# Kernel tuning notes

Measured on AMD Instinct MI355X. Metric: run time of the kernel, lower is better.

Reference implementation:

```python
import jax, jax.numpy as jnp
import numpy as np

B, T, N, H = 4096, 128, 128, 128  # batch, timesteps, input_size, encoder_num_hidden
EPS = 1e-5  # BatchNorm1d eps


def setup_inputs() -> dict:
    key = jax.random.key(0)
    ks = jax.random.split(key, 12)
    g = lambda k, shp, s=0.088: jax.random.normal(k, shp, dtype=jnp.float32) * s  # ~1/sqrt(H)
    return {
        "X": jax.random.normal(ks[0], (B, T, N), dtype=jnp.float32),
        "attn_w": g(ks[1], (2 * H + T,)),
        "attn_b": jnp.zeros((), jnp.float32),
        "bn_gamma": jnp.ones((N,), jnp.float32),
        "bn_beta": jnp.zeros((N,), jnp.float32),
        "W_ih0": g(ks[2], (4 * H, N)),
        "W_hh0": g(ks[3], (4 * H, H)),
        "b_ih0": g(ks[4], (4 * H,)),
        "b_hh0": g(ks[5], (4 * H,)),
        "W_ih1": g(ks[6], (4 * H, H)),
        "W_hh1": g(ks[7], (4 * H, H)),
        "b_ih1": g(ks[8], (4 * H,)),
        "b_hh1": g(ks[9], (4 * H,)),
    }


def _lstm_cell(x, h, c, W_ih, W_hh, b):
    # torch gate order: i, f, g, o
    gates = x @ W_ih.T + h @ W_hh.T + b  # (B, 4H)
    i, f, gg, o = jnp.split(gates, 4, axis=-1)
    c_new = jax.nn.sigmoid(f) * c + jax.nn.sigmoid(i) * jnp.tanh(gg)
    h_new = jax.nn.sigmoid(o) * jnp.tanh(c_new)
    return h_new, c_new


def reference(X, attn_w, attn_b, bn_gamma, bn_beta,
              W_ih0, W_hh0, b_ih0, b_hh0, W_ih1, W_hh1, b_ih1, b_hh1):
    # Attention input per step is cat(h_top repeat, s_top repeat, X^T) -> Linear(2H+T -> 1).
    # The X^T contribution is time-invariant; precompute it once.
    w_h, w_s, w_x = attn_w[:H], attn_w[H:2 * H], attn_w[2 * H:]
    Xp = jnp.transpose(X, (0, 2, 1))            # (B, N, T) driving-series view
    score_x = Xp @ w_x + attn_b                 # (B, N)
    b0 = b_ih0 + b_hh0
    b1 = b_ih1 + b_hh1

    def step(carry, x_t):
        h0, c0, h1, c1 = carry                  # layer0/layer1 hidden & cell (B, H)
        # h_n[-1], s_n[-1] are broadcast identically over all N features
        scores = score_x + (h1 @ w_h)[:, None] + (c1 @ w_s)[:, None]  # (B, N)
        alpha = jax.nn.softmax(scores, axis=1)
        x_tilde = alpha * x_t                   # (B, N)
        # BatchNorm1d in training mode: batch statistics over dim 0
        mean = jnp.mean(x_tilde, axis=0)
        var = jnp.var(x_tilde, axis=0)
        xb = (x_tilde - mean) * jax.lax.rsqrt(var + EPS) * bn_gamma + bn_beta
        # 2-layer LSTM single step (dropout inactive in eval)
        h0n, c0n = _lstm_cell(xb, h0, c0, W_ih0, W_hh0, b0)
        h1n, c1n = _lstm_cell(h0n, h1, c1, W_ih1, W_hh1, b1)
        return (h0n, c0n, h1n, c1n), (x_tilde, h1n)

    zeros = jnp.zeros((B, H), X.dtype)
    init = (zeros, zeros, zeros, zeros)
    Xt = jnp.transpose(X, (1, 0, 2))            # (T, B, N) for scan
    _, (xt_seq, he_seq) = jax.lax.scan(step, init, Xt)
    X_tilde = jnp.transpose(xt_seq, (1, 0, 2))   # (B, T, N)
    X_encoded = jnp.transpose(he_seq, (1, 0, 2)) # (B, T, H)
    return X_tilde, X_encoded
```

## Files before the change

### kernel.cpp

```cpp
#include <hip/hip_runtime.h>
#include <cstdint>
#include <cstddef>

#define B_ 4096
#define T_ 128
#define N_ 128
#define H_ 128
#define G4_ 512
#define KC_ 256
#define EPS_ 1e-5f

#define RPB_ 16
#define NB_ 256
#define W0K_ 128
#define W0P_ 136

#define KB2_ 256
#define ROWS2_ 16

typedef _Float16 f16x8 __attribute__((ext_vector_type(8)));
typedef _Float16 f16x4 __attribute__((ext_vector_type(4)));
typedef float f32x4 __attribute__((ext_vector_type(4)));

__device__ __forceinline__ float sigm_(float x) { return 1.f / (1.f + __expf(-x)); }
__device__ __forceinline__ float tanh_(float x) {
  float ax = fabsf(x);
  float e = __expf(-2.f * ax);
  float t = (1.f - e) / (1.f + e);
  return copysignf(t, x);
}

__global__ void k0_prep(const float* __restrict__ Wih0, const float* __restrict__ Whh0,
                        const float* __restrict__ bih0, const float* __restrict__ bhh0,
                        const float* __restrict__ Wih1, const float* __restrict__ Whh1,
                        const float* __restrict__ bih1, const float* __restrict__ bhh1,
                        _Float16* __restrict__ Wpack, float* __restrict__ bpack) {
  int idx = blockIdx.x * blockDim.x + threadIdx.x;
  if (idx < 2 * G4_ * KC_) {
    int k = idx & (KC_ - 1);
    int j = (idx >> 8) & (G4_ - 1);
    int l = idx >> 17;
    const float* Wih = l ? Wih1 : Wih0;
    const float* Whh = l ? Whh1 : Whh0;
    float v = (k < N_) ? Wih[j * N_ + k] : Whh[j * N_ + (k - N_)];
    Wpack[idx] = (_Float16)v;
  }
  if (idx < 2 * G4_) {
    int j = idx & (G4_ - 1);
    bpack[idx] = (idx >> 9) ? (bih1[j] + bhh1[j]) : (bih0[j] + bhh0[j]);
  }
}

__global__ __launch_bounds__(512, 1) void k12_fused(
    const float* __restrict__ X, const float* __restrict__ attn_w,
    const float* __restrict__ attn_b, float* __restrict__ out0,
    float* __restrict__ psum, float* __restrict__ psq) {
  __shared__ float xs[2 * T_ * N_];
  __shared__ float wx[T_];
  __shared__ float redS[4][N_];
  __shared__ float redM[8], redE[8];
  const int tid = threadIdx.x;
  const int blk = blockIdx.x;
  const int n = tid & 127;
  const int tq = tid >> 7;
  const int wv = tid >> 6;
  const int row0 = blk * ROWS2_;
  if (tid < T_) wx[tid] = attn_w[2 * H_ + tid];
  const float ab = attn_b[0];

  float sum[32], sq[32];
#pragma unroll
  for (int i = 0; i < 32; ++i) { sum[i] = 0.f; sq[i] = 0.f; }

  {
    const float* xb = X + (size_t)row0 * T_ * N_;
#pragma unroll
    for (int i = 0; i < 8; ++i) {
      int fi = ((i << 9) + tid) << 2;
      *(f32x4*)&xs[fi] = *(const f32x4*)&xb[fi];
    }
  }

  int buf = 0;
  for (int rb = 0; rb < ROWS2_; ++rb) {
    __syncthreads();
    const float* xcur = xs + (buf << 14);

    f32x4 stg[8];
    if (rb + 1 < ROWS2_) {
      const float* xb1 = X + (size_t)(row0 + rb + 1) * T_ * N_;
#pragma unroll
      for (int i = 0; i < 8; ++i)
        stg[i] = *(const f32x4*)&xb1[((i << 9) + tid) << 2];
    }

    float s = 0.f;
#pragma unroll
    for (int tt = 0; tt < 32; ++tt) {
      int t = (tq << 5) + tt;
      s = fmaf(xcur[t * N_ + n], wx[t], s);
    }
    redS[tq][n] = s;
    __syncthreads();
    s = redS[0][n] + redS[1][n] + redS[2][n] + redS[3][n] + ab;

    float m = s;
#pragma unroll
    for (int off = 32; off >= 1; off >>= 1) m = fmaxf(m, __shfl_xor(m, off));
    if ((tid & 63) == 0) redM[wv] = m;
    __syncthreads();
    m = fmaxf(fmaxf(fmaxf(redM[0], redM[1]), fmaxf(redM[2], redM[3])),
              fmaxf(fmaxf(redM[4], redM[5]), fmaxf(redM[6], redM[7])));
    float e = __expf(s - m);
    float sm = e;
#pragma unroll
    for (int off = 32; off >= 1; off >>= 1) sm += __shfl_xor(sm, off);
    if ((tid & 63) == 0) redE[wv] = sm;
    __syncthreads();
    sm = redE[0] + redE[1];
    const float alpha = e / sm;

    if (rb + 1 < ROWS2_) {
      float* xnx = xs + ((buf ^ 1) << 14);
#pragma unroll
      for (int i = 0; i < 8; ++i)
        *(f32x4*)&xnx[((i << 9) + tid) << 2] = stg[i];
    }

    const size_t b = (size_t)(row0 + rb);
#pragma unroll
    for (int tt = 0; tt < 32; ++tt) {
      int t = (tq << 5) + tt;
      float v = alpha * xcur[t * N_ + n];
      sum[tt] += v;
      sq[tt] += v * v;
      out0[(b * T_ + t) * N_ + n] = v;
    }
    buf ^= 1;
  }

  float* pbs = psum + ((size_t)blk << 14) + (tq << 5) * N_ + n;
  float* pbq = psq + ((size_t)blk << 14) + (tq << 5) * N_ + n;
#pragma unroll
  for (int tt = 0; tt < 32; ++tt) {
    pbs[tt * N_] = sum[tt];
    pbq[tt * N_] = sq[tt];
  }
}

__global__ void k3r(const float* __restrict__ psum, const float* __restrict__ psq,
                    const float* __restrict__ gamma, const float* __restrict__ beta,
                    float* __restrict__ scale, float* __restrict__ shift) {
  __shared__ float rs[2][N_], rq[2][N_];
  const int t = blockIdx.x;
  const int tid = threadIdx.x;
  const int n = tid & 127;
  const int hb = tid >> 7;
  const size_t off = (size_t)t * N_ + n;
  float s = 0.f, q = 0.f;
#pragma unroll 4
  for (int i = 0; i < 128; ++i) {
    size_t o = ((size_t)((hb << 7) + i) << 14) + off;
    s += psum[o];
    q += psq[o];
  }
  rs[hb][n] = s;
  rq[hb][n] = q;
  __syncthreads();
  if (hb == 0) {
    s = rs[0][n] + rs[1][n];
    q = rq[0][n] + rq[1][n];
    float mean = s * (1.f / B_);
    float var = q * (1.f / B_) - mean * mean;
    float rstd = rsqrtf(var + EPS_);
    float g = gamma[n];
    scale[t * N_ + n] = rstd * g;
    shift[t * N_ + n] = beta[n] - mean * rstd * g;
  }
}

__global__ __launch_bounds__(512, 2) void k4_recur(
    const float* __restrict__ xt , const _Float16* __restrict__ Wpack,
    const float* __restrict__ bpack, const float* __restrict__ scale,
    const float* __restrict__ shift, float* __restrict__ out1) {
  __shared__ _Float16 W0l[G4_][W0P_];
  __shared__ _Float16 A0[RPB_][264];
  __shared__ _Float16 A1[RPB_][264];

  const int tid = threadIdx.x;
  const int w = tid >> 6;
  const int lane = tid & 63;
  const int quad = lane >> 4;
  const int l16 = lane & 15;
  const int nb = blockIdx.x;
  const int col = (w << 4) + l16;

  {
    const _Float16* src = Wpack + (size_t)tid * KC_;
#pragma unroll
    for (int kk = 0; kk < W0K_; kk += 8)
      *(f16x8*)&W0l[tid][kk] = *(const f16x8*)&src[kk];
  }

  f16x8 w1[4][8];
#pragma unroll
  for (int g = 0; g < 4; ++g) {
    const _Float16* src = Wpack + (size_t)(G4_ + (g << 7) + col) * KC_ + (quad << 3);
#pragma unroll
    for (int kb = 0; kb < 8; ++kb) w1[g][kb] = *(const f16x8*)&src[kb << 5];
  }

  float bia0[4], bia1[4];
#pragma unroll
  for (int g = 0; g < 4; ++g) {
    bia0[g] = bpack[(g << 7) + col];
    bia1[g] = bpack[G4_ + (g << 7) + col];
  }

  float c0[4], c1[4];
#pragma unroll
  for (int e = 0; e < 4; ++e) { c0[e] = 0.f; c1[e] = 0.f; }

  const int sr = tid >> 5;
  const int sc = (tid & 31) << 2;
  const size_t browbase = (size_t)(nb * RPB_ + sr) * T_;

  {
    f32x4 xv = *(const f32x4*)(xt + (browbase + 0) * N_ + sc);
    f32x4 s4 = *(const f32x4*)(scale + sc);
    f32x4 h4 = *(const f32x4*)(shift + sc);
    f16x4 hv;
#pragma unroll
    for (int e = 0; e < 4; ++e) hv[e] = (_Float16)fmaf(xv[e], s4[e], h4[e]);
    *(f16x4*)&A0[sr][sc] = hv;
    f16x4 z = {};
    *(f16x4*)&A0[sr][N_ + sc] = z;
    *(f16x4*)&A1[sr][N_ + sc] = z;
  }
  __syncthreads();

  for (int t = 0; t < T_; ++t) {
    f32x4 xn = {};
    if (t + 1 < T_) xn = *(const f32x4*)(xt + (browbase + t + 1) * N_ + sc);

    f32x4 acc[4] = {};
#pragma unroll
    for (int kb = 0; kb < 8; ++kb) {
      f16x8 a = *(const f16x8*)&A0[l16][(kb << 5) + (quad << 3)];
      if (kb < 4) {
#pragma unroll
        for (int g = 0; g < 4; ++g) {
          f16x8 bf = *(const f16x8*)&W0l[(g << 7) + col][(kb << 5) + (quad << 3)];
          acc[g] = __builtin_amdgcn_mfma_f32_16x16x32_f16(a, bf, acc[g], 0, 0, 0);
        }
      } else {
#pragma unroll
        for (int g = 0; g < 4; ++g) {
          f16x8 bf = *(const f16x8*)(Wpack + (size_t)((g << 7) + col) * KC_ +
                                     (kb << 5) + (quad << 3));
          acc[g] = __builtin_amdgcn_mfma_f32_16x16x32_f16(a, bf, acc[g], 0, 0, 0);
        }
      }
    }

    _Float16 h0h[4];
#pragma unroll
    for (int e = 0; e < 4; ++e) {
      float ig = acc[0][e] + bia0[0];
      float fg = acc[1][e] + bia0[1];
      float gg = acc[2][e] + bia0[2];
      float og = acc[3][e] + bia0[3];
      float cn = sigm_(fg) * c0[e] + sigm_(ig) * tanh_(gg);
      c0[e] = cn;
      h0h[e] = (_Float16)(sigm_(og) * tanh_(cn));
    }
    __syncthreads();
#pragma unroll
    for (int e = 0; e < 4; ++e) {
      A0[(quad << 2) + e][N_ + col] = h0h[e];
      A1[(quad << 2) + e][col] = h0h[e];
    }
    __syncthreads();

    f16x8 a1[8];
#pragma unroll
    for (int kb = 0; kb < 4; ++kb) {
      a1[kb] = *(const f16x8*)&A1[l16][(kb << 5) + (quad << 3)];
      a1[4 + kb] = *(const f16x8*)&A1[l16][128 + (kb << 5) + (quad << 3)];
    }
    f32x4 acc1[4] = {};
#pragma unroll
    for (int kb = 0; kb < 8; ++kb) {
#pragma unroll
      for (int g = 0; g < 4; ++g)
        acc1[g] = __builtin_amdgcn_mfma_f32_16x16x32_f16(a1[kb], w1[g][kb], acc1[g], 0, 0, 0);
    }

    _Float16 h1h[4];
#pragma unroll
    for (int e = 0; e < 4; ++e) {
      float ig = acc1[0][e] + bia1[0];
      float fg = acc1[1][e] + bia1[1];
      float gg = acc1[2][e] + bia1[2];
      float og = acc1[3][e] + bia1[3];
      float cn = sigm_(fg) * c1[e] + sigm_(ig) * tanh_(gg);
      c1[e] = cn;
      float hn = sigm_(og) * tanh_(cn);
      h1h[e] = (_Float16)hn;
      out1[((size_t)(nb * RPB_ + (quad << 2) + e) * T_ + t) * H_ + col] = hn;
    }
    __syncthreads();
#pragma unroll
    for (int e = 0; e < 4; ++e)
      A1[(quad << 2) + e][N_ + col] = h1h[e];
    if (t + 1 < T_) {
      f32x4 s4 = *(const f32x4*)(scale + (t + 1) * N_ + sc);
      f32x4 h4 = *(const f32x4*)(shift + (t + 1) * N_ + sc);
      f16x4 hv;
#pragma unroll
      for (int e = 0; e < 4; ++e) hv[e] = (_Float16)fmaf(xn[e], s4[e], h4[e]);
      *(f16x4*)&A0[sr][sc] = hv;
    }
    __syncthreads();
  }
}

extern "C" void kernel_launch(void* const* d_in, const int* in_sizes, int n_in,
                              void* d_out, int out_size, void* d_ws, size_t ws_size,
                              hipStream_t stream) {
  const float* X = (const float*)d_in[0];
  const float* attnw = (const float*)d_in[1];
  const float* attnb = (const float*)d_in[2];
  const float* gamma = (const float*)d_in[3];
  const float* beta = (const float*)d_in[4];
  const float* Wih0 = (const float*)d_in[5];
  const float* Whh0 = (const float*)d_in[6];
  const float* bih0 = (const float*)d_in[7];
  const float* bhh0 = (const float*)d_in[8];
  const float* Wih1 = (const float*)d_in[9];
  const float* Whh1 = (const float*)d_in[10];
  const float* bih1 = (const float*)d_in[11];
  const float* bhh1 = (const float*)d_in[12];

  float* out0 = (float*)d_out;
  float* out1 = out0 + (size_t)B_ * T_ * N_;

  float* psum = out1;
  float* psq = out1 + ((size_t)KB2_ << 14);

  float* ws = (float*)d_ws;
  float* scale = ws;
  float* shift = scale + T_ * N_;
  float* bpack = shift + T_ * N_;
  _Float16* Wpack = (_Float16*)(bpack + 2 * G4_);

  k0_prep<<<1024, 256, 0, stream>>>(Wih0, Whh0, bih0, bhh0, Wih1, Whh1, bih1, bhh1,
                                    Wpack, bpack);
  k12_fused<<<KB2_, 512, 0, stream>>>(X, attnw, attnb, out0, psum, psq);
  k3r<<<T_, 256, 0, stream>>>(psum, psq, gamma, beta, scale, shift);
  k4_recur<<<NB_, 512, 0, stream>>>(out0, Wpack, bpack, scale, shift, out1);
}
```

Measured before the change: 1.332 ms.

## Software-pipeline LSTM layers so layer1 step t overlaps layer0 step t+1

Restructures the recurrent loop into a prologue, a steady-state loop and an epilogue. Layer-1 of step t and layer-0 of step t+1 now run in the same iteration, since they depend on the same h0 and on independent state. This halves the block barriers per timestep and gives the scheduler two independent MFMA chains to interleave, hiding MFMA and LDS latency. The cost is higher register pressure from holding two accumulator sets at once, plus a few extra prefetched loads.

```diff
diff --git a/kernel.cpp b/kernel.cpp
--- a/kernel.cpp
+++ b/kernel.cpp
@@ -29,6 +29,8 @@
   float t = (1.f - e) / (1.f + e);
   return copysignf(t, x);
 }
+
+#define MFMA16(a, b, c) __builtin_amdgcn_mfma_f32_16x16x32_f16((a), (b), (c), 0, 0, 0)
 
 __global__ void k0_prep(const float* __restrict__ Wih0, const float* __restrict__ Whh0,
                         const float* __restrict__ bih0, const float* __restrict__ bhh0,
@@ -224,6 +226,7 @@
   const int sr = tid >> 5;
   const int sc = (tid & 31) << 2;
   const size_t browbase = (size_t)(nb * RPB_ + sr) * T_;
+  const size_t orowbase = (size_t)(nb * RPB_ + (quad << 2)) * T_;
 
   {
     f32x4 xv = *(const f32x4*)(xt + (browbase + 0) * N_ + sc);
@@ -239,10 +242,7 @@
   }
   __syncthreads();
 
-  for (int t = 0; t < T_; ++t) {
-    f32x4 xn = {};
-    if (t + 1 < T_) xn = *(const f32x4*)(xt + (browbase + t + 1) * N_ + sc);
-
+  {
     f32x4 acc[4] = {};
 #pragma unroll
     for (int kb = 0; kb < 8; ++kb) {
@@ -251,18 +251,17 @@
 #pragma unroll
         for (int g = 0; g < 4; ++g) {
           f16x8 bf = *(const f16x8*)&W0l[(g << 7) + col][(kb << 5) + (quad << 3)];
-          acc[g] = __builtin_amdgcn_mfma_f32_16x16x32_f16(a, bf, acc[g], 0, 0, 0);
+          acc[g] = MFMA16(a, bf, acc[g]);
         }
       } else {
 #pragma unroll
         for (int g = 0; g < 4; ++g) {
           f16x8 bf = *(const f16x8*)(Wpack + (size_t)((g << 7) + col) * KC_ +
                                      (kb << 5) + (quad << 3));
-          acc[g] = __builtin_amdgcn_mfma_f32_16x16x32_f16(a, bf, acc[g], 0, 0, 0);
+          acc[g] = MFMA16(a, bf, acc[g]);
         }
       }
     }
-
     _Float16 h0h[4];
 #pragma unroll
     for (int e = 0; e < 4; ++e) {
@@ -277,10 +276,28 @@
     __syncthreads();
 #pragma unroll
     for (int e = 0; e < 4; ++e) {
+      A1[(quad << 2) + e][col] = h0h[e];
       A0[(quad << 2) + e][N_ + col] = h0h[e];
-      A1[(quad << 2) + e][col] = h0h[e];
-    }
-    __syncthreads();
+    }
+    {
+      f32x4 xv = *(const f32x4*)(xt + (browbase + 1) * N_ + sc);
+      f32x4 s4 = *(const f32x4*)(scale + 1 * N_ + sc);
+      f32x4 h4 = *(const f32x4*)(shift + 1 * N_ + sc);
+      f16x4 hv;
+#pragma unroll
+      for (int e = 0; e < 4; ++e) hv[e] = (_Float16)fmaf(xv[e], s4[e], h4[e]);
+      *(f16x4*)&A0[sr][sc] = hv;
+    }
+    __syncthreads();
+  }
+
+  for (int t = 0; t < T_ - 1; ++t) {
+    f32x4 xn = {}, scn = {}, shn = {};
+    if (t + 2 < T_) {
+      xn = *(const f32x4*)(xt + (browbase + t + 2) * N_ + sc);
+      scn = *(const f32x4*)(scale + (t + 2) * N_ + sc);
+      shn = *(const f32x4*)(shift + (t + 2) * N_ + sc);
+    }
 
     f16x8 a1[8];
 #pragma unroll
@@ -292,8 +309,27 @@
 #pragma unroll
     for (int kb = 0; kb < 8; ++kb) {
 #pragma unroll
-      for (int g = 0; g < 4; ++g)
-        acc1[g] = __builtin_amdgcn_mfma_f32_16x16x32_f16(a1[kb], w1[g][kb], acc1[g], 0, 0, 0);
+      for (int g = 0; g < 4; ++g) acc1[g] = MFMA16(a1[kb], w1[g][kb], acc1[g]);
+    }
+
+    f32x4 acc[4] = {};
+#pragma unroll
+    for (int kb = 0; kb < 8; ++kb) {
+      f16x8 a = *(const f16x8*)&A0[l16][(kb << 5) + (quad << 3)];
+      if (kb < 4) {
+#pragma unroll
+        for (int g = 0; g < 4; ++g) {
+          f16x8 bf = *(const f16x8*)&W0l[(g << 7) + col][(kb << 5) + (quad << 3)];
+          acc[g] = MFMA16(a, bf, acc[g]);
+        }
+      } else {
+#pragma unroll
+        for (int g = 0; g < 4; ++g) {
+          f16x8 bf = *(const f16x8*)(Wpack + (size_t)((g << 7) + col) * KC_ +
+                                     (kb << 5) + (quad << 3));
+          acc[g] = MFMA16(a, bf, acc[g]);
+        }
+      }
     }
 
     _Float16 h1h[4];
@@ -307,21 +343,58 @@
       c1[e] = cn;
       float hn = sigm_(og) * tanh_(cn);
       h1h[e] = (_Float16)hn;
-      out1[((size_t)(nb * RPB_ + (quad << 2) + e) * T_ + t) * H_ + col] = hn;
-    }
-    __syncthreads();
-#pragma unroll
-    for (int e = 0; e < 4; ++e)
+      out1[(orowbase + (size_t)e * T_ + t) * H_ + col] = hn;
+    }
+    _Float16 h0h[4];
+#pragma unroll
+    for (int e = 0; e < 4; ++e) {
+      float ig = acc[0][e] + bia0[0];
+      float fg = acc[1][e] + bia0[1];
+      float gg = acc[2][e] + bia0[2];
+      float og = acc[3][e] + bia0[3];
+      float cn = sigm_(fg) * c0[e] + sigm_(ig) * tanh_(gg);
+      c0[e] = cn;
+      h0h[e] = (_Float16)(sigm_(og) * tanh_(cn));
+    }
+    __syncthreads();
+#pragma unroll
+    for (int e = 0; e < 4; ++e) {
+      A1[(quad << 2) + e][col] = h0h[e];
       A1[(quad << 2) + e][N_ + col] = h1h[e];
-    if (t + 1 < T_) {
-      f32x4 s4 = *(const f32x4*)(scale + (t + 1) * N_ + sc);
-      f32x4 h4 = *(const f32x4*)(shift + (t + 1) * N_ + sc);
+      A0[(quad << 2) + e][N_ + col] = h0h[e];
+    }
+    if (t + 2 < T_) {
       f16x4 hv;
 #pragma unroll
-      for (int e = 0; e < 4; ++e) hv[e] = (_Float16)fmaf(xn[e], s4[e], h4[e]);
+      for (int e = 0; e < 4; ++e) hv[e] = (_Float16)fmaf(xn[e], scn[e], shn[e]);
       *(f16x4*)&A0[sr][sc] = hv;
     }
     __syncthreads();
+  }
+
+  {
+    f16x8 a1[8];
+#pragma unroll
+    for (int kb = 0; kb < 4; ++kb) {
+      a1[kb] = *(const f16x8*)&A1[l16][(kb << 5) + (quad << 3)];
+      a1[4 + kb] = *(const f16x8*)&A1[l16][128 + (kb << 5) + (quad << 3)];
+    }
+    f32x4 acc1[4] = {};
+#pragma unroll
+    for (int kb = 0; kb < 8; ++kb) {
+#pragma unroll
+      for (int g = 0; g < 4; ++g) acc1[g] = MFMA16(a1[kb], w1[g][kb], acc1[g]);
+    }
+#pragma unroll
+    for (int e = 0; e < 4; ++e) {
+      float ig = acc1[0][e] + bia1[0];
+      float fg = acc1[1][e] + bia1[1];
+      float gg = acc1[2][e] + bia1[2];
+      float og = acc1[3][e] + bia1[3];
+      float cn = sigm_(fg) * c1[e] + sigm_(ig) * tanh_(gg);
+      float hn = sigm_(og) * tanh_(cn);
+      out1[(orowbase + (size_t)e * T_ + (T_ - 1)) * H_ + col] = hn;
+    }
   }
 }
 
```

Result: slower. 1.499 ms (+12.6%).

## Restructure LSTM recurrence to two barriers per step with skewed layer-1 epilogue

Applied to the files above, without the earlier changes.

Splits the shared activation tiles into separate XB/H0/H0n/H1 buffers, double-buffering the layer-0 hidden state. The layer-1 gate nonlinearity and output store are deferred to the start of the next step, so each timestep needs two barriers instead of four. The layer-0 weight tile in LDS is stored with an XOR swizzle instead of padding, to avoid bank conflicts. Scale and shift loads for the next step are also issued earlier. The price is more LDS buffers, a peeled final epilogue, and more complex indexing.

```diff
diff --git a/kernel.cpp b/kernel.cpp
--- a/kernel.cpp
+++ b/kernel.cpp
@@ -13,7 +13,7 @@
 #define RPB_ 16
 #define NB_ 256
 #define W0K_ 128
-#define W0P_ 136
+#define AP_ 136
 
 #define KB2_ 256
 #define ROWS2_ 16
@@ -29,6 +29,8 @@
   float t = (1.f - e) / (1.f + e);
   return copysignf(t, x);
 }
+
+#define MFMA16(a, b, c) __builtin_amdgcn_mfma_f32_16x16x32_f16((a), (b), (c), 0, 0, 0)
 
 __global__ void k0_prep(const float* __restrict__ Wih0, const float* __restrict__ Whh0,
                         const float* __restrict__ bih0, const float* __restrict__ bhh0,
@@ -183,9 +185,11 @@
     const float* __restrict__ xt , const _Float16* __restrict__ Wpack,
     const float* __restrict__ bpack, const float* __restrict__ scale,
     const float* __restrict__ shift, float* __restrict__ out1) {
-  __shared__ _Float16 W0l[G4_][W0P_];
-  __shared__ _Float16 A0[RPB_][264];
-  __shared__ _Float16 A1[RPB_][264];
+  __shared__ _Float16 W0l[G4_ * 128];
+  __shared__ _Float16 XB[RPB_][AP_];
+  __shared__ _Float16 H0[2][RPB_][AP_];
+  __shared__ _Float16 H0n[RPB_][AP_];
+  __shared__ _Float16 H1[RPB_][AP_];
 
   const int tid = threadIdx.x;
   const int w = tid >> 6;
@@ -197,9 +201,11 @@
 
   {
     const _Float16* src = Wpack + (size_t)tid * KC_;
-#pragma unroll
-    for (int kk = 0; kk < W0K_; kk += 8)
-      *(f16x8*)&W0l[tid][kk] = *(const f16x8*)&src[kk];
+    char* dst = (char*)W0l + tid * 256;
+    const int sw = (tid & 7) << 4;
+#pragma unroll
+    for (int o = 0; o < 256; o += 16)
+      *(f16x8*)(dst + (o ^ sw)) = *(const f16x8*)((const char*)src + o);
   }
 
   f16x8 w1[4][8];
@@ -220,10 +226,13 @@
   float c0[4], c1[4];
 #pragma unroll
   for (int e = 0; e < 4; ++e) { c0[e] = 0.f; c1[e] = 0.f; }
+  f32x4 acc1[4] = {};
 
   const int sr = tid >> 5;
   const int sc = (tid & 31) << 2;
   const size_t browbase = (size_t)(nb * RPB_ + sr) * T_;
+  const size_t orowbase = (size_t)(nb * RPB_ + (quad << 2)) * T_;
+  const int swr = (l16 & 7) << 4;
 
   {
     f32x4 xv = *(const f32x4*)(xt + (browbase + 0) * N_ + sc);
@@ -232,33 +241,61 @@
     f16x4 hv;
 #pragma unroll
     for (int e = 0; e < 4; ++e) hv[e] = (_Float16)fmaf(xv[e], s4[e], h4[e]);
-    *(f16x4*)&A0[sr][sc] = hv;
+    *(f16x4*)&XB[sr][sc] = hv;
     f16x4 z = {};
-    *(f16x4*)&A0[sr][N_ + sc] = z;
-    *(f16x4*)&A1[sr][N_ + sc] = z;
+    *(f16x4*)&H0[0][sr][sc] = z;
+    *(f16x4*)&H1[sr][sc] = z;
   }
   __syncthreads();
 
   for (int t = 0; t < T_; ++t) {
-    f32x4 xn = {};
-    if (t + 1 < T_) xn = *(const f32x4*)(xt + (browbase + t + 1) * N_ + sc);
+    const int cb = t & 1, cbn = cb ^ 1;
+
+    f32x4 xn = {}, scn = {}, shn = {};
+    if (t + 1 < T_) {
+      xn = *(const f32x4*)(xt + (browbase + t + 1) * N_ + sc);
+      scn = *(const f32x4*)(scale + (t + 1) * N_ + sc);
+      shn = *(const f32x4*)(shift + (t + 1) * N_ + sc);
+    }
+
+    if (t > 0) {
+      _Float16 h1h[4];
+#pragma unroll
+      for (int e = 0; e < 4; ++e) {
+        float ig = acc1[0][e] + bia1[0];
+        float fg = acc1[1][e] + bia1[1];
+        float gg = acc1[2][e] + bia1[2];
+        float og = acc1[3][e] + bia1[3];
+        float cn = sigm_(fg) * c1[e] + sigm_(ig) * tanh_(gg);
+        c1[e] = cn;
+        float hn = sigm_(og) * tanh_(cn);
+        h1h[e] = (_Float16)hn;
+        out1[(orowbase + (size_t)e * T_ + (t - 1)) * H_ + col] = hn;
+      }
+#pragma unroll
+      for (int e = 0; e < 4; ++e)
+        H1[(quad << 2) + e][col] = h1h[e];
+    }
 
     f32x4 acc[4] = {};
 #pragma unroll
     for (int kb = 0; kb < 8; ++kb) {
-      f16x8 a = *(const f16x8*)&A0[l16][(kb << 5) + (quad << 3)];
+      f16x8 a = (kb < 4)
+                    ? *(const f16x8*)&XB[l16][(kb << 5) + (quad << 3)]
+                    : *(const f16x8*)&H0[cb][l16][((kb - 4) << 5) + (quad << 3)];
       if (kb < 4) {
 #pragma unroll
         for (int g = 0; g < 4; ++g) {
-          f16x8 bf = *(const f16x8*)&W0l[(g << 7) + col][(kb << 5) + (quad << 3)];
-          acc[g] = __builtin_amdgcn_mfma_f32_16x16x32_f16(a, bf, acc[g], 0, 0, 0);
+          const char* wr = (const char*)W0l + (((g << 7) + col) << 8);
+          f16x8 bf = *(const f16x8*)(wr + (((kb << 6) | (quad << 4)) ^ swr));
+          acc[g] = MFMA16(a, bf, acc[g]);
         }
       } else {
 #pragma unroll
         for (int g = 0; g < 4; ++g) {
           f16x8 bf = *(const f16x8*)(Wpack + (size_t)((g << 7) + col) * KC_ +
                                      (kb << 5) + (quad << 3));
-          acc[g] = __builtin_amdgcn_mfma_f32_16x16x32_f16(a, bf, acc[g], 0, 0, 0);
+          acc[g] = MFMA16(a, bf, acc[g]);
         }
       }
     }
@@ -274,29 +311,34 @@
       c0[e] = cn;
       h0h[e] = (_Float16)(sigm_(og) * tanh_(cn));
     }
-    __syncthreads();
 #pragma unroll
     for (int e = 0; e < 4; ++e) {
-      A0[(quad << 2) + e][N_ + col] = h0h[e];
-      A1[(quad << 2) + e][col] = h0h[e];
-    }
-    __syncthreads();
-
-    f16x8 a1[8];
-#pragma unroll
-    for (int kb = 0; kb < 4; ++kb) {
-      a1[kb] = *(const f16x8*)&A1[l16][(kb << 5) + (quad << 3)];
-      a1[4 + kb] = *(const f16x8*)&A1[l16][128 + (kb << 5) + (quad << 3)];
-    }
-    f32x4 acc1[4] = {};
+      H0n[(quad << 2) + e][col] = h0h[e];
+      H0[cbn][(quad << 2) + e][col] = h0h[e];
+    }
+    __syncthreads();
+
+#pragma unroll
+    for (int g = 0; g < 4; ++g) acc1[g] = (f32x4){0.f, 0.f, 0.f, 0.f};
 #pragma unroll
     for (int kb = 0; kb < 8; ++kb) {
-#pragma unroll
-      for (int g = 0; g < 4; ++g)
-        acc1[g] = __builtin_amdgcn_mfma_f32_16x16x32_f16(a1[kb], w1[g][kb], acc1[g], 0, 0, 0);
-    }
-
-    _Float16 h1h[4];
+      f16x8 a = (kb < 4)
+                    ? *(const f16x8*)&H0n[l16][(kb << 5) + (quad << 3)]
+                    : *(const f16x8*)&H1[l16][((kb - 4) << 5) + (quad << 3)];
+#pragma unroll
+      for (int g = 0; g < 4; ++g) acc1[g] = MFMA16(a, w1[g][kb], acc1[g]);
+    }
+
+    if (t + 1 < T_) {
+      f16x4 hv;
+#pragma unroll
+      for (int e = 0; e < 4; ++e) hv[e] = (_Float16)fmaf(xn[e], scn[e], shn[e]);
+      *(f16x4*)&XB[sr][sc] = hv;
+    }
+    __syncthreads();
+  }
+
+  {
 #pragma unroll
     for (int e = 0; e < 4; ++e) {
       float ig = acc1[0][e] + bia1[0];
@@ -304,24 +346,9 @@
       float gg = acc1[2][e] + bia1[2];
       float og = acc1[3][e] + bia1[3];
       float cn = sigm_(fg) * c1[e] + sigm_(ig) * tanh_(gg);
-      c1[e] = cn;
       float hn = sigm_(og) * tanh_(cn);
-      h1h[e] = (_Float16)hn;
-      out1[((size_t)(nb * RPB_ + (quad << 2) + e) * T_ + t) * H_ + col] = hn;
-    }
-    __syncthreads();
-#pragma unroll
-    for (int e = 0; e < 4; ++e)
-      A1[(quad << 2) + e][N_ + col] = h1h[e];
-    if (t + 1 < T_) {
-      f32x4 s4 = *(const f32x4*)(scale + (t + 1) * N_ + sc);
-      f32x4 h4 = *(const f32x4*)(shift + (t + 1) * N_ + sc);
-      f16x4 hv;
-#pragma unroll
-      for (int e = 0; e < 4; ++e) hv[e] = (_Float16)fmaf(xn[e], s4[e], h4[e]);
-      *(f16x4*)&A0[sr][sc] = hv;
-    }
-    __syncthreads();
+      out1[(orowbase + (size_t)e * T_ + (T_ - 1)) * H_ + col] = hn;
+    }
   }
 }
 
```

After: 1.355 ms. About the same (+1.8%).
